# Optimization experiments

Hardware: AMD Instinct MI355X
Metric: run time of the kernel (lower is better)

Reference implementation:

```python
import jax, jax.numpy as jnp
import numpy as np

HIDDEN = 1024
HEADS = 16
HEAD_DIM = HIDDEN // HEADS


def setup_inputs() -> dict:
    key = jax.random.key(0)
    ks = jax.random.split(key, 9)
    s = 1.0 / np.sqrt(HIDDEN)  # nn.Linear default init scale (uniform bound)
    def lin(kw, kb):
        W = jax.random.uniform(kw, (HIDDEN, HIDDEN), jnp.float32, -s, s)
        b = jax.random.uniform(kb, (HIDDEN,), jnp.float32, -s, s)
        return W, b
    Wq, bq = lin(ks[0], ks[1])
    Wk, bk = lin(ks[2], ks[3])
    Wv, bv = lin(ks[4], ks[5])
    Wo, bo = lin(ks[6], ks[7])
    x = jax.random.normal(ks[8], (2, 2048, HIDDEN), jnp.float32)
    return {"x": x, "Wq": Wq, "bq": bq, "Wk": Wk, "bk": bk,
            "Wv": Wv, "bv": bv, "Wo": Wo, "bo": bo}


def reference(x, Wq, bq, Wk, bk, Wv, bv, Wo, bo):
    B, S, _ = x.shape
    # projections (torch Linear: y = x @ W.T + b)
    def proj(W, b):
        y = jnp.einsum('bsh,oh->bso', x, W) + b
        return y.reshape(B, S, HEADS, HEAD_DIM)
    q = proj(Wq, bq)  # [B,S,H,D]
    k = proj(Wk, bk)
    v = proj(Wv, bv)
    scale = 1.0 / np.sqrt(HEAD_DIM)
    scores = jnp.einsum('bqhd,bkhd->bhqk', q, k) * scale  # [B,H,S,S]
    probs = jax.nn.softmax(scores, axis=-1)
    out = jnp.einsum('bhqk,bkhd->bqhd', probs, v).reshape(B, S, HIDDEN)
    return jnp.einsum('bsh,oh->bso', out, Wo) + bo
```

## Files before the change

kernel.cpp:

```cpp
#include <hip/hip_runtime.h>
#include <hip/hip_bf16.h>
#include <stdint.h>

#define HIDDEN 1024
#define SEQ 2048
#define BATCH 2
#define HEADS 16
#define HDIM 64
#define M_TOK (BATCH * SEQ)

using bf16_t = __bf16;
typedef __attribute__((ext_vector_type(8))) __bf16 bf16x8;
typedef __attribute__((ext_vector_type(4))) float f32x4;

__device__ __forceinline__ bf16_t tobf(float f) {
  uint32_t u = __builtin_bit_cast(uint32_t, f);
  u += 0x7FFFu + ((u >> 16) & 1u);
  uint16_t h = (uint16_t)(u >> 16);
  return __builtin_bit_cast(bf16_t, h);
}

__device__ __forceinline__ void async_cp16(const bf16_t* g, bf16_t* l) {
  __builtin_amdgcn_global_load_lds(
      (const __attribute__((address_space(1))) uint32_t*)g,
      (__attribute__((address_space(3))) uint32_t*)l, 16, 0, 0);
}

__global__ __launch_bounds__(256) void k_convert(const float* __restrict__ src,
                                                 bf16_t* __restrict__ dst, int n) {
  int i = (blockIdx.x * 256 + threadIdx.x) * 4;
  if (i >= n) return;
  float4 v = *(const float4*)(src + i);
  union { bf16_t b[4]; uint64_t u; } o;
  o.b[0] = tobf(v.x); o.b[1] = tobf(v.y); o.b[2] = tobf(v.z); o.b[3] = tobf(v.w);
  *(uint64_t*)(dst + i) = o.u;
}

__global__ __launch_bounds__(256) void k_convert4(
    const float* __restrict__ s0, const float* __restrict__ s1,
    const float* __restrict__ s2, const float* __restrict__ s3,
    bf16_t* __restrict__ d0, bf16_t* __restrict__ d1,
    bf16_t* __restrict__ d2, bf16_t* __restrict__ d3) {
  const int wsel = blockIdx.y;
  const float* src = (wsel == 0) ? s0 : (wsel == 1) ? s1 : (wsel == 2) ? s2 : s3;
  bf16_t* dst = (wsel == 0) ? d0 : (wsel == 1) ? d1 : (wsel == 2) ? d2 : d3;
  int i = (blockIdx.x * 256 + threadIdx.x) * 4;
  float4 v = *(const float4*)(src + i);
  union { bf16_t b[4]; uint64_t u; } o;
  o.b[0] = tobf(v.x); o.b[1] = tobf(v.y); o.b[2] = tobf(v.z); o.b[3] = tobf(v.w);
  *(uint64_t*)(dst + i) = o.u;
}

template <int MODE>
__device__ __forceinline__ void gemm_bt_body(const bf16_t* __restrict__ A,
                                             const bf16_t* __restrict__ Bw,
                                             const float* __restrict__ bias,
                                             void* __restrict__ dst,
                                             bf16_t* As, bf16_t* Bs) {
  constexpr int K = HIDDEN;
  const int tid = threadIdx.x;
  const int lane = tid & 63;
  const int w = tid >> 6;
  const int wr = w >> 1, wc = w & 1;
  const int lr = lane & 15, lg = lane >> 4;
  const int m0 = blockIdx.x * 128;
  const int n0 = blockIdx.y * 128;

  f32x4 acc[4][4];
#pragma unroll
  for (int i = 0; i < 4; ++i)
#pragma unroll
    for (int j = 0; j < 4; ++j) acc[i][j] = f32x4{0.f, 0.f, 0.f, 0.f};

  for (int k0 = 0; k0 < K; k0 += 32) {
#pragma unroll
    for (int i = 0; i < 2; ++i) {
      int c = w * 128 + i * 64 + lane;
      int row = c >> 2, kc = c & 3;
      async_cp16(A + (size_t)(m0 + row) * K + k0 + kc * 8, As + c * 8);
      async_cp16(Bw + (size_t)(n0 + row) * K + k0 + kc * 8, Bs + c * 8);
    }
    __syncthreads();
    bf16x8 af[4], bfr[4];
#pragma unroll
    for (int mi = 0; mi < 4; ++mi)
      af[mi] = *(const bf16x8*)(As + (wr * 64 + mi * 16 + lr) * 32 + lg * 8);
#pragma unroll
    for (int ni = 0; ni < 4; ++ni)
      bfr[ni] = *(const bf16x8*)(Bs + (wc * 64 + ni * 16 + lr) * 32 + lg * 8);
#pragma unroll
    for (int mi = 0; mi < 4; ++mi)
#pragma unroll
      for (int ni = 0; ni < 4; ++ni)
        acc[mi][ni] = __builtin_amdgcn_mfma_f32_16x16x32_bf16(af[mi], bfr[ni], acc[mi][ni], 0, 0, 0);
    __syncthreads();
  }

#pragma unroll
  for (int ni = 0; ni < 4; ++ni) {
    int col = n0 + wc * 64 + ni * 16 + lr;
    float bv = bias[col];
#pragma unroll
    for (int mi = 0; mi < 4; ++mi) {
#pragma unroll
      for (int r = 0; r < 4; ++r) {
        int m = m0 + wr * 64 + mi * 16 + lg * 4 + r;
        float v = acc[mi][ni][r] + bv;
        if (MODE == 0) {
          int b = m >> 11, s = m & (SEQ - 1);
          int h = col >> 6, d = col & 63;
          ((bf16_t*)dst)[(((size_t)(b * HEADS + h) * SEQ) + s) * HDIM + d] = tobf(v);
        } else {
          ((float*)dst)[(size_t)m * HIDDEN + col] = v;
        }
      }
    }
  }
}

__global__ __launch_bounds__(256) void k_gemm_qkv(
    const bf16_t* __restrict__ A,
    const bf16_t* __restrict__ Wqb, const bf16_t* __restrict__ Wkb,
    const bf16_t* __restrict__ Wvb,
    const float* __restrict__ bq, const float* __restrict__ bk,
    const float* __restrict__ bv,
    bf16_t* __restrict__ Qb, bf16_t* __restrict__ Kb, bf16_t* __restrict__ Vb) {
  __shared__ bf16_t As[128 * 32];
  __shared__ bf16_t Bs[128 * 32];
  const int z = blockIdx.z;
  const bf16_t* Bw = (z == 0) ? Wqb : (z == 1) ? Wkb : Wvb;
  const float* bias = (z == 0) ? bq : (z == 1) ? bk : bv;
  bf16_t* dst = (z == 0) ? Qb : (z == 1) ? Kb : Vb;
  gemm_bt_body<0>(A, Bw, bias, dst, As, Bs);
}

__global__ __launch_bounds__(256) void k_gemm_out(const bf16_t* __restrict__ A,
                                                  const bf16_t* __restrict__ Bw,
                                                  const float* __restrict__ bias,
                                                  float* __restrict__ dst) {
  __shared__ bf16_t As[128 * 32];
  __shared__ bf16_t Bs[128 * 32];
  gemm_bt_body<1>(A, Bw, bias, dst, As, Bs);
}

__global__ __launch_bounds__(256) void k_attn(const bf16_t* __restrict__ Q,
                                              const bf16_t* __restrict__ Kk,
                                              const bf16_t* __restrict__ V,
                                              bf16_t* __restrict__ AO) {
  __shared__ bf16_t Vt[64 * 64];
  __shared__ bf16_t Pl[4][16 * 64];
  const int tid = threadIdx.x;
  const int lane = tid & 63;
  const int w = tid >> 6;
  const int lr = lane & 15, lg = lane >> 4;

  const int lin = blockIdx.y * gridDim.x + blockIdx.x;
  const int wk = ((lin & 7) << 7) + (lin >> 3);
  const int bx = wk & 31;
  const int bh = wk >> 5;

  const int q0 = bx * 64 + w * 16;
  const bf16_t* Qh = Q + (size_t)bh * SEQ * HDIM;
  const bf16_t* Kh = Kk + (size_t)bh * SEQ * HDIM;
  const bf16_t* Vh = V + (size_t)bh * SEQ * HDIM;

  const float qscale = 0.125f * 1.44269504088896f;
  bf16x8 aq[2];
#pragma unroll
  for (int dc = 0; dc < 2; ++dc) {
    bf16x8 t = *(const bf16x8*)(Qh + (size_t)(q0 + lr) * HDIM + dc * 32 + lg * 8);
#pragma unroll
    for (int j = 0; j < 8; ++j) t[j] = tobf((float)t[j] * qscale);
    aq[dc] = t;
  }

  bf16x8 vone;
#pragma unroll
  for (int j = 0; j < 8; ++j) vone[j] = tobf(1.0f);

  float mrow[4];
  f32x4 acc[4];
  f32x4 accd = f32x4{0.f, 0.f, 0.f, 0.f};
#pragma unroll
  for (int r = 0; r < 4; ++r) mrow[r] = -1e30f;
#pragma unroll
  for (int fc = 0; fc < 4; ++fc) acc[fc] = f32x4{0.f, 0.f, 0.f, 0.f};

  for (int kt = 0; kt < SEQ / 64; ++kt) {
    const int kr0 = kt * 64;
    __syncthreads();
    {
      int k = tid >> 2, d0 = (tid & 3) * 16;
      const bf16_t* vp = Vh + (size_t)(kr0 + k) * HDIM + d0;
#pragma unroll
      for (int half = 0; half < 2; ++half) {
        bf16x8 vv = *(const bf16x8*)(vp + half * 8);
#pragma unroll
        for (int j = 0; j < 8; ++j) {
          int d = d0 + half * 8 + j;
          Vt[d * 64 + (((k >> 3) ^ (d & 7)) * 8) + (k & 7)] = vv[j];
        }
      }
    }
    __syncthreads();

    f32x4 sf[4];
    __builtin_amdgcn_s_setprio(1);
#pragma unroll
    for (int fc = 0; fc < 4; ++fc) {
      f32x4 a = f32x4{0.f, 0.f, 0.f, 0.f};
      int kr = kr0 + fc * 16 + lr;
#pragma unroll
      for (int dc = 0; dc < 2; ++dc) {
        bf16x8 bk = *(const bf16x8*)(Kh + (size_t)kr * HDIM + dc * 32 + lg * 8);
        a = __builtin_amdgcn_mfma_f32_16x16x32_bf16(aq[dc], bk, a, 0, 0, 0);
      }
      sf[fc] = a;
    }
    __builtin_amdgcn_s_setprio(0);

    float pmax[4];
#pragma unroll
    for (int r = 0; r < 4; ++r)
      pmax[r] = fmaxf(fmaxf(sf[0][r], sf[1][r]), fmaxf(sf[2][r], sf[3][r]));
    int ok = (pmax[0] <= mrow[0] + 8.f) && (pmax[1] <= mrow[1] + 8.f) &&
             (pmax[2] <= mrow[2] + 8.f) && (pmax[3] <= mrow[3] + 8.f);
    if (!__all(ok)) {
#pragma unroll
      for (int r = 0; r < 4; ++r) {
        float mx = pmax[r];
        mx = fmaxf(mx, __shfl_xor(mx, 1));
        mx = fmaxf(mx, __shfl_xor(mx, 2));
        mx = fmaxf(mx, __shfl_xor(mx, 4));
        mx = fmaxf(mx, __shfl_xor(mx, 8));
        float mn = fmaxf(mrow[r], mx);
        float sc = exp2f(mrow[r] - mn);
        mrow[r] = mn;
        accd[r] *= sc;
#pragma unroll
        for (int fc = 0; fc < 4; ++fc) acc[fc][r] *= sc;
      }
    }
    float pv[4][4];
#pragma unroll
    for (int r = 0; r < 4; ++r)
#pragma unroll
      for (int fc = 0; fc < 4; ++fc) pv[fc][r] = exp2f(sf[fc][r] - mrow[r]);

#pragma unroll
    for (int fc = 0; fc < 4; ++fc) {
      int col = fc * 16 + lr;
#pragma unroll
      for (int r = 0; r < 4; ++r) {
        int row = lg * 4 + r;
        Pl[w][row * 64 + (((col >> 3) ^ (row & 7)) * 8) + (col & 7)] = tobf(pv[fc][r]);
      }
    }

    bf16x8 pa[2];
#pragma unroll
    for (int kc = 0; kc < 2; ++kc) {
      int swz = (kc * 4 + lg) ^ (lr & 7);
      pa[kc] = *(const bf16x8*)(&Pl[w][lr * 64 + swz * 8]);
    }
    __builtin_amdgcn_s_setprio(1);
#pragma unroll
    for (int fc = 0; fc < 4; ++fc) {
      int d = fc * 16 + lr;
#pragma unroll
      for (int kc = 0; kc < 2; ++kc) {
        int swz = (kc * 4 + lg) ^ (d & 7);
        bf16x8 bv = *(const bf16x8*)(&Vt[d * 64 + swz * 8]);
        acc[fc] = __builtin_amdgcn_mfma_f32_16x16x32_bf16(pa[kc], bv, acc[fc], 0, 0, 0);
      }
    }
    accd = __builtin_amdgcn_mfma_f32_16x16x32_bf16(pa[0], vone, accd, 0, 0, 0);
    accd = __builtin_amdgcn_mfma_f32_16x16x32_bf16(pa[1], vone, accd, 0, 0, 0);
    __builtin_amdgcn_s_setprio(0);
  }

  const int b = bh >> 4, h = bh & 15;
#pragma unroll
  for (int fc = 0; fc < 4; ++fc) {
#pragma unroll
    for (int r = 0; r < 4; ++r) {
      int srow = q0 + lg * 4 + r;
      float o = acc[fc][r] / accd[r];
      AO[((size_t)(b * SEQ + srow)) * HIDDEN + h * HDIM + fc * 16 + lr] = tobf(o);
    }
  }
}

extern "C" void kernel_launch(void* const* d_in, const int* in_sizes, int n_in,
                              void* d_out, int out_size, void* d_ws, size_t ws_size,
                              hipStream_t stream) {
  const float* x  = (const float*)d_in[0];
  const float* Wq = (const float*)d_in[1];
  const float* bq = (const float*)d_in[2];
  const float* Wk = (const float*)d_in[3];
  const float* bk = (const float*)d_in[4];
  const float* Wv = (const float*)d_in[5];
  const float* bv = (const float*)d_in[6];
  const float* Wo = (const float*)d_in[7];
  const float* bo = (const float*)d_in[8];

  char* ws = (char*)d_ws;
  const size_t XB = (size_t)M_TOK * HIDDEN * 2;
  const size_t WB = (size_t)HIDDEN * HIDDEN * 2;
  bf16_t* xb  = (bf16_t*)(ws);
  bf16_t* Wqb = (bf16_t*)(ws + XB);
  bf16_t* Wkb = (bf16_t*)(ws + XB + 1 * WB);
  bf16_t* Wvb = (bf16_t*)(ws + XB + 2 * WB);
  bf16_t* Wob = (bf16_t*)(ws + XB + 3 * WB);
  bf16_t* Qb  = (bf16_t*)(ws + XB + 4 * WB);
  bf16_t* Kb  = (bf16_t*)(ws + 2 * XB + 4 * WB);
  bf16_t* Vb  = (bf16_t*)(ws + 3 * XB + 4 * WB);
  bf16_t* AOb = (bf16_t*)(ws + 4 * XB + 4 * WB);

  k_convert<<<(M_TOK * HIDDEN) / 1024, 256, 0, stream>>>(x, xb, M_TOK * HIDDEN);
  k_convert4<<<dim3((HIDDEN * HIDDEN) / 1024, 4), 256, 0, stream>>>(
      Wq, Wk, Wv, Wo, Wqb, Wkb, Wvb, Wob);

  dim3 gg(M_TOK / 128, HIDDEN / 128);
  k_gemm_qkv<<<dim3(M_TOK / 128, HIDDEN / 128, 3), 256, 0, stream>>>(
      xb, Wqb, Wkb, Wvb, bq, bk, bv, Qb, Kb, Vb);

  k_attn<<<dim3(SEQ / 64, BATCH * HEADS), 256, 0, stream>>>(Qb, Kb, Vb, AOb);

  k_gemm_out<<<gg, 256, 0, stream>>>(AOb, Wob, bo, (float*)d_out);
}
```

Baseline: 196.3 us.

## Split attention key range across two wave groups with log-sum-exp merge

Doubles the attention block to 512 threads. Two groups of four waves each process half of the key sequence for the same 64 query rows, and each group stages its own V tile in shared memory. At the end, partial accumulators, denominators and row maxima are passed through shared memory and combined with rescaling before the output is written. This is meant to add parallelism and latency hiding per query tile. The cost is extra shared memory, a merge phase with barriers, and possibly fewer resident blocks per CU.

```diff
diff --git a/kernel.cpp b/kernel.cpp
--- a/kernel.cpp
+++ b/kernel.cpp
@@ -143,15 +143,17 @@
   gemm_bt_body<1>(A, Bw, bias, dst, As, Bs);
 }
 
-__global__ __launch_bounds__(256) void k_attn(const bf16_t* __restrict__ Q,
+__global__ __launch_bounds__(512) void k_attn(const bf16_t* __restrict__ Q,
                                               const bf16_t* __restrict__ Kk,
                                               const bf16_t* __restrict__ V,
                                               bf16_t* __restrict__ AO) {
-  __shared__ bf16_t Vt[64 * 64];
-  __shared__ bf16_t Pl[4][16 * 64];
+  __shared__ bf16_t Vt[2][64 * 64];
+  __shared__ bf16_t Pl[8][16 * 64];
   const int tid = threadIdx.x;
   const int lane = tid & 63;
   const int w = tid >> 6;
+  const int g = w >> 2;
+  const int rw = w & 3;
   const int lr = lane & 15, lg = lane >> 4;
 
   const int lin = blockIdx.y * gridDim.x + blockIdx.x;
@@ -159,7 +161,7 @@
   const int bx = wk & 31;
   const int bh = wk >> 5;
 
-  const int q0 = bx * 64 + w * 16;
+  const int q0 = bx * 64 + rw * 16;
   const bf16_t* Qh = Q + (size_t)bh * SEQ * HDIM;
   const bf16_t* Kh = Kk + (size_t)bh * SEQ * HDIM;
   const bf16_t* Vh = V + (size_t)bh * SEQ * HDIM;
@@ -186,19 +188,22 @@
 #pragma unroll
   for (int fc = 0; fc < 4; ++fc) acc[fc] = f32x4{0.f, 0.f, 0.f, 0.f};
 
-  for (int kt = 0; kt < SEQ / 64; ++kt) {
-    const int kr0 = kt * 64;
+  const int HT = (SEQ / 64) / 2;
+
+  for (int it = 0; it < HT; ++it) {
+    const int kr0 = (g * HT + it) * 64;
     __syncthreads();
     {
-      int k = tid >> 2, d0 = (tid & 3) * 16;
-      const bf16_t* vp = Vh + (size_t)(kr0 + k) * HDIM + d0;
+      int t2 = tid >> 8, tid2 = tid & 255;
+      int k = tid2 >> 2, d0 = (tid2 & 3) * 16;
+      const bf16_t* vp = Vh + (size_t)((t2 * HT + it) * 64 + k) * HDIM + d0;
 #pragma unroll
       for (int half = 0; half < 2; ++half) {
         bf16x8 vv = *(const bf16x8*)(vp + half * 8);
 #pragma unroll
         for (int j = 0; j < 8; ++j) {
           int d = d0 + half * 8 + j;
-          Vt[d * 64 + (((k >> 3) ^ (d & 7)) * 8) + (k & 7)] = vv[j];
+          Vt[t2][d * 64 + (((k >> 3) ^ (d & 7)) * 8) + (k & 7)] = vv[j];
         }
       }
     }
@@ -270,7 +275,7 @@
 #pragma unroll
       for (int kc = 0; kc < 2; ++kc) {
         int swz = (kc * 4 + lg) ^ (d & 7);
-        bf16x8 bv = *(const bf16x8*)(&Vt[d * 64 + swz * 8]);
+        bf16x8 bv = *(const bf16x8*)(&Vt[g][d * 64 + swz * 8]);
         acc[fc] = __builtin_amdgcn_mfma_f32_16x16x32_bf16(pa[kc], bv, acc[fc], 0, 0, 0);
       }
     }
@@ -279,14 +284,42 @@
     __builtin_amdgcn_s_setprio(0);
   }
 
+  float* Mg = (float*)&Vt[0][0];
   const int b = bh >> 4, h = bh & 15;
 #pragma unroll
-  for (int fc = 0; fc < 4; ++fc) {
-#pragma unroll
-    for (int r = 0; r < 4; ++r) {
-      int srow = q0 + lg * 4 + r;
-      float o = acc[fc][r] / accd[r];
-      AO[((size_t)(b * SEQ + srow)) * HIDDEN + h * HDIM + fc * 16 + lr] = tobf(o);
+  for (int ph = 0; ph < 2; ++ph) {
+    __syncthreads();
+    if (g == 1 && (w & 2) == (ph << 1)) {
+      float* dst = Mg + ((w & 1) * 64 + lane) * 25;
+#pragma unroll
+      for (int fc = 0; fc < 4; ++fc)
+#pragma unroll
+        for (int r = 0; r < 4; ++r) dst[fc * 4 + r] = acc[fc][r];
+#pragma unroll
+      for (int r = 0; r < 4; ++r) { dst[16 + r] = accd[r]; dst[20 + r] = mrow[r]; }
+    }
+    __syncthreads();
+    if (g == 0 && (w & 2) == (ph << 1)) {
+      const float* src = Mg + ((w & 1) * 64 + lane) * 25;
+#pragma unroll
+      for (int r = 0; r < 4; ++r) {
+        float mB = src[20 + r], dB = src[16 + r];
+        float m2 = fmaxf(mrow[r], mB);
+        float sA = exp2f(mrow[r] - m2), sB = exp2f(mB - m2);
+        accd[r] = accd[r] * sA + dB * sB;
+#pragma unroll
+        for (int fc = 0; fc < 4; ++fc)
+          acc[fc][r] = acc[fc][r] * sA + src[fc * 4 + r] * sB;
+      }
+#pragma unroll
+      for (int fc = 0; fc < 4; ++fc) {
+#pragma unroll
+        for (int r = 0; r < 4; ++r) {
+          int srow = q0 + lg * 4 + r;
+          float o = acc[fc][r] / accd[r];
+          AO[((size_t)(b * SEQ + srow)) * HIDDEN + h * HDIM + fc * 16 + lr] = tobf(o);
+        }
+      }
     }
   }
 }
@@ -325,7 +358,7 @@
   k_gemm_qkv<<<dim3(M_TOK / 128, HIDDEN / 128, 3), 256, 0, stream>>>(
       xb, Wqb, Wkb, Wvb, bq, bk, bv, Qb, Kb, Vb);
 
-  k_attn<<<dim3(SEQ / 64, BATCH * HEADS), 256, 0, stream>>>(Qb, Kb, Vb, AOb);
+  k_attn<<<dim3(SEQ / 64, BATCH * HEADS), 512, 0, stream>>>(Qb, Kb, Vb, AOb);
 
   k_gemm_out<<<gg, 256, 0, stream>>>(AOb, Wob, bo, (float*)d_out);
 }
```

Measured after the change: 228.7 us. +16.5%, slower.
